# Performance work log

Measured on AMD Instinct MI355X. Metric: run time of the kernel, lower is better.

The kernel has to match this reference:

```python
import jax, jax.numpy as jnp
import numpy as np

B, S, DIM, H, HD, K, DEPTH = 2, 2048, 1024, 16, 64, 64, 8
SCALE = 1.0 / np.sqrt(HD)


def _build_cantor_routes(seq_len: int, k: int, depth: int) -> np.ndarray:
    # Vectorized version of CantorAttention._build_cantor_routes
    pos = np.arange(seq_len, dtype=np.float64)
    x = pos / max(1, seq_len - 1)
    x = np.clip(x, 1e-06, 1.0 - 1e-06)
    cantor = np.zeros(seq_len, dtype=np.float64)
    factor = 0.5
    for _ in range(depth):
        x = x * 3.0
        digit = np.floor(x)
        x = x - digit
        cantor += factor * (digit == 2.0)
        factor *= 0.5
    cantor = cantor.astype(np.float32)
    # k nearest positions in Cantor space for each position
    dist = np.abs(cantor[:, None] - cantor[None, :])  # [S, S]
    routes = np.argsort(dist, axis=1, kind='stable')[:, :k]  # [S, k]
    return routes.astype(np.int32)


def setup_inputs() -> dict:
    key = jax.random.key(0)
    k1, k2, k3, k4, k5 = jax.random.split(key, 5)
    s = 1.0 / np.sqrt(DIM)
    return {
        'x': jax.random.normal(k1, (B, S, DIM), dtype=jnp.float32),
        'w_qkv': jax.random.normal(k2, (3 * DIM, DIM), dtype=jnp.float32) * s,
        'b_qkv': jax.random.normal(k3, (3 * DIM,), dtype=jnp.float32) * 0.01,
        'w_out': jax.random.normal(k4, (DIM, DIM), dtype=jnp.float32) * s,
        'b_out': jax.random.normal(k5, (DIM,), dtype=jnp.float32) * 0.01,
        'routes': jnp.asarray(_build_cantor_routes(S, K, DEPTH)),
    }


def reference(x, w_qkv, b_qkv, w_out, b_out, routes):
    b, s, _ = x.shape
    # QKV projection (torch Linear: y = x @ W.T + b)
    qkv = x @ w_qkv.T + b_qkv                       # [B, S, 3*DIM]
    qkv = qkv.reshape(b, s, 3, H, HD).transpose(2, 0, 3, 1, 4)  # [3, B, H, S, HD]
    q, k, v = qkv[0], qkv[1], qkv[2]                # each [B, H, S, HD]
    # Gather k/v at Cantor neighbor routes: [B, H, S, K, HD]
    k_g = jnp.take(k, routes, axis=2)
    v_g = jnp.take(v, routes, axis=2)
    scores = jnp.einsum('bhqd,bhqkd->bhqk', q, k_g) * SCALE
    attn = jax.nn.softmax(scores, axis=-1)
    out = jnp.einsum('bhqk,bhqkd->bhqd', attn, v_g)  # [B, H, S, HD]
    out = out.transpose(0, 2, 1, 3).reshape(b, s, DIM)
    return out @ w_out.T + b_out
```

## Files before the change

kernel.cpp:

```cpp
#include <hip/hip_runtime.h>

#define BQ   2
#define SQ   2048
#define DIMQ 1024
#define HQ   16
#define HDQ  64
#define KQ   64
#define QKV_STRIDE (3 * DIMQ)

typedef __attribute__((ext_vector_type(8))) short short8;
typedef __attribute__((ext_vector_type(4))) float floatx4;

typedef const __attribute__((address_space(1))) unsigned short* gas_t;
typedef __attribute__((address_space(3))) unsigned short* las_t;

__device__ __forceinline__ unsigned short f2b(float f) {
    union { float f; unsigned int u; } x; x.f = f;
    unsigned int r = x.u + 0x7fffu + ((x.u >> 16) & 1u);
    return (unsigned short)(r >> 16);
}
__device__ __forceinline__ float b2f(unsigned short u) {
    union { unsigned int u; float f; } x; x.u = ((unsigned int)u) << 16;
    return x.f;
}

__global__ __launch_bounds__(256) void cast3_f32_bf16(const float* __restrict__ s0, unsigned short* __restrict__ d0, int n0,
                                                      const float* __restrict__ s1, unsigned short* __restrict__ d1, int n1,
                                                      const float* __restrict__ s2, unsigned short* __restrict__ d2, int n2) {
    int i = blockIdx.x * blockDim.x + threadIdx.x;
    const float* s; unsigned short* d;
    if (i < n0)                { s = s0; d = d0; }
    else if (i < n0 + n1)      { s = s1; d = d1; i -= n0; }
    else if (i < n0 + n1 + n2) { s = s2; d = d2; i -= n0 + n1; }
    else return;
    float4 v = ((const float4*)s)[i];
    ushort4 o;
    o.x = f2b(v.x); o.y = f2b(v.y); o.z = f2b(v.z); o.w = f2b(v.w);
    ((ushort4*)d)[i] = o;
}

template <int BM, int BN, typename CT>
__global__ __launch_bounds__(256) void gemm_bf16_nt(const unsigned short* __restrict__ A,
                                                    const unsigned short* __restrict__ B,
                                                    const float* __restrict__ bias,
                                                    CT* __restrict__ C,
                                                    int M, int N, int K) {
    constexpr int MI = BM / 32;
    constexpr int NJ = BN / 32;
    __shared__ unsigned short As[BM * 64];
    __shared__ unsigned short Bs[BN * 64];

    const int tid  = threadIdx.x;
    const int lane = tid & 63;
    const int wv   = tid >> 6;
    const int wm   = (wv >> 1) * (BM / 2);
    const int wn   = (wv & 1) * (BN / 2);
    const int fr   = lane & 15;
    const int fq   = lane >> 4;

    const int m0 = blockIdx.y * BM;
    const int n0 = blockIdx.x * BN;

    floatx4 acc[MI][NJ];
#pragma unroll
    for (int i = 0; i < MI; ++i)
#pragma unroll
        for (int j = 0; j < NJ; ++j) acc[i][j] = (floatx4)(0.f);

    const unsigned short* Ab = A + (size_t)m0 * K;
    const unsigned short* Bb = B + (size_t)n0 * K;

    for (int k0 = 0; k0 < K; k0 += 64) {
#pragma unroll
        for (int c = 0; c < (BM + BN) * 8; c += 256) {
            const int cc = c + tid;
            if (cc < BM * 8) {
                const int row = cc >> 3;
                const int kc  = ((cc & 7) ^ (row & 7)) << 3;
                __builtin_amdgcn_global_load_lds(
                    (gas_t)(Ab + (size_t)row * K + k0 + kc),
                    (las_t)&As[cc * 8], 16, 0, 0);
            } else {
                const int c2  = cc - BM * 8;
                const int row = c2 >> 3;
                const int kc  = ((c2 & 7) ^ (row & 7)) << 3;
                __builtin_amdgcn_global_load_lds(
                    (gas_t)(Bb + (size_t)row * K + k0 + kc),
                    (las_t)&Bs[c2 * 8], 16, 0, 0);
            }
        }
        __syncthreads();

#pragma unroll
        for (int ks = 0; ks < 2; ++ks) {
            short8 af[MI], bf[NJ];
#pragma unroll
            for (int i = 0; i < MI; ++i) {
                const int row = wm + i * 16 + fr;
                const int pos = (ks * 4 + fq) ^ (row & 7);
                af[i] = *(const short8*)&As[row * 64 + pos * 8];
            }
#pragma unroll
            for (int j = 0; j < NJ; ++j) {
                const int row = wn + j * 16 + fr;
                const int pos = (ks * 4 + fq) ^ (row & 7);
                bf[j] = *(const short8*)&Bs[row * 64 + pos * 8];
            }
#pragma unroll
            for (int i = 0; i < MI; ++i)
#pragma unroll
                for (int j = 0; j < NJ; ++j)
                    acc[i][j] = __builtin_amdgcn_mfma_f32_16x16x32_bf16(af[i], bf[j], acc[i][j], 0, 0, 0);
        }
        __syncthreads();
    }

    float bv[NJ];
#pragma unroll
    for (int j = 0; j < NJ; ++j) bv[j] = bias[n0 + wn + j * 16 + fr];
#pragma unroll
    for (int i = 0; i < MI; ++i) {
#pragma unroll
        for (int r = 0; r < 4; ++r) {
            const size_t row = (size_t)(m0 + wm + i * 16 + fq * 4 + r);
#pragma unroll
            for (int j = 0; j < NJ; ++j) {
                const float v = acc[i][j][r] + bv[j];
                if constexpr (sizeof(CT) == 2)
                    C[row * N + n0 + wn + j * 16 + fr] = (CT)f2b(v);
                else
                    C[row * N + n0 + wn + j * 16 + fr] = (CT)v;
            }
        }
    }
}

__global__ __launch_bounds__(256) void attn_kernel(const unsigned short* __restrict__ qkv,
                                                   const int* __restrict__ routes,
                                                   unsigned short* __restrict__ out) {
    __shared__ int   r_s[KQ];
    __shared__ float m_s[128], l_s[128];
    __shared__ float o_part[8][128];

    const int t  = threadIdx.x;
    const int id = blockIdx.x;
    const int bq = (id & 7) * 512 + (id >> 3);
    const int b  = bq >> 11;
    const int q  = bq & 2047;

    if (t < KQ) r_s[t] = routes[q * KQ + t];

    const int g  = t >> 7;
    const int th = t & 127;
    const int h  = th >> 3;
    const int d0 = (t & 7) * 8;

    float qf[8];
    {
        const short8 q8 = *(const short8*)&qkv[((size_t)bq * 3) * DIMQ + h * HDQ + d0];
#pragma unroll
        for (int e = 0; e < 8; ++e) qf[e] = b2f((unsigned short)q8[e]);
    }
    __syncthreads();

    const size_t baseK = ((size_t)b * SQ * 3 + 1) * DIMQ + h * HDQ + d0;
    const size_t baseV = ((size_t)b * SQ * 3 + 2) * DIMQ + h * HDQ + d0;

    float m = -1e30f, l = 0.f;
    float o[8];
#pragma unroll
    for (int e = 0; e < 8; ++e) o[e] = 0.f;

#pragma unroll 4
    for (int jj = 0; jj < KQ / 2; ++jj) {
        const int j = jj * 2 + g;
        const size_t roff = (size_t)r_s[j] * QKV_STRIDE;
        const short8 k8 = *(const short8*)&qkv[baseK + roff];
        const short8 v8 = *(const short8*)&qkv[baseV + roff];
        float p = 0.f;
#pragma unroll
        for (int e = 0; e < 8; ++e) p += qf[e] * b2f((unsigned short)k8[e]);
        p += __shfl_xor(p, 1, 64);
        p += __shfl_xor(p, 2, 64);
        p += __shfl_xor(p, 4, 64);
        const float s  = p * 0.125f;
        const float mn = fmaxf(m, s);
        const float al = __expf(m - mn);
        const float pe = __expf(s - mn);
        l = l * al + pe;
#pragma unroll
        for (int e = 0; e < 8; ++e) o[e] = o[e] * al + pe * b2f((unsigned short)v8[e]);
        m = mn;
    }

    if (g == 1) {
        m_s[th] = m; l_s[th] = l;
#pragma unroll
        for (int e = 0; e < 8; ++e) o_part[e][th] = o[e];
    }
    __syncthreads();
    if (g == 0) {
        const float m1 = m_s[th], l1 = l_s[th];
        const float mm = fmaxf(m, m1);
        const float a0 = __expf(m - mm);
        const float a1 = __expf(m1 - mm);
        const float inv = 1.0f / (l * a0 + l1 * a1);
        float oo[8];
#pragma unroll
        for (int e = 0; e < 8; ++e) oo[e] = (o[e] * a0 + o_part[e][th] * a1) * inv;
        ushort4 lo, hi;
        lo.x = f2b(oo[0]); lo.y = f2b(oo[1]); lo.z = f2b(oo[2]); lo.w = f2b(oo[3]);
        hi.x = f2b(oo[4]); hi.y = f2b(oo[5]); hi.z = f2b(oo[6]); hi.w = f2b(oo[7]);
        ushort4* dst = (ushort4*)&out[(size_t)bq * DIMQ + h * HDQ + d0];
        dst[0] = lo; dst[1] = hi;
    }
}

extern "C" void kernel_launch(void* const* d_in, const int* in_sizes, int n_in,
                              void* d_out, int out_size, void* d_ws, size_t ws_size,
                              hipStream_t stream) {
    const float* x      = (const float*)d_in[0];
    const float* w_qkv  = (const float*)d_in[1];
    const float* b_qkv  = (const float*)d_in[2];
    const float* w_out  = (const float*)d_in[3];
    const float* b_out  = (const float*)d_in[4];
    const int*   routes = (const int*)d_in[5];
    float* out = (float*)d_out;

    char* ws = (char*)d_ws;
    unsigned short* qkvb  = (unsigned short*)ws;
    unsigned short* xb    = (unsigned short*)(ws + 25165824);
    unsigned short* attnb = xb;
    unsigned short* wqb   = (unsigned short*)(ws + 33554432);
    unsigned short* wob   = (unsigned short*)(ws + 39845888);

    const int M = BQ * SQ;
    dim3 blk(256);

    {
        const int n0 = M * DIMQ / 4, n1 = 3 * DIMQ * DIMQ / 4, n2 = DIMQ * DIMQ / 4;
        cast3_f32_bf16<<<(n0 + n1 + n2 + 255) / 256, blk, 0, stream>>>(
            x, xb, n0, w_qkv, wqb, n1, w_out, wob, n2);
    }

    gemm_bf16_nt<128, 128, unsigned short><<<dim3(3 * DIMQ / 128, M / 128), blk, 0, stream>>>(
        xb, wqb, b_qkv, qkvb, M, 3 * DIMQ, DIMQ);

    attn_kernel<<<BQ * SQ, blk, 0, stream>>>(qkvb, routes, attnb);

    gemm_bf16_nt<128, 64, float><<<dim3(DIMQ / 64, M / 128), blk, 0, stream>>>(
        attnb, wob, b_out, out, M, DIMQ, DIMQ);
}
```

Before: 189.5 us.

## Order attention queries by Cantor rank and split softmax into two passes

Adds two small kernels that compute Cantor coordinates and a rank permutation of query positions on device. The attention kernel then processes queries in Cantor order, so neighbouring blocks gather overlapping K/V rows and cache reuse should improve. The online softmax is replaced by three phases: score computation into shared memory, a block-wide normalisation, then a weighted V sum. This removes the per-step rescaling exps but adds two block barriers and two extra kernel launches, one of which is an O(S^2) rank loop.

Measured after the change: 299.7 us. 1.58x slower.

```diff
diff --git a/kernel.cpp b/kernel.cpp
--- a/kernel.cpp
+++ b/kernel.cpp
@@ -22,6 +22,35 @@
 __device__ __forceinline__ float b2f(unsigned short u) {
     union { unsigned int u; float f; } x; x.u = ((unsigned int)u) << 16;
     return x.f;
+}
+
+__global__ __launch_bounds__(256) void cantor_vals(double* __restrict__ cant) {
+    const int q = blockIdx.x * 256 + threadIdx.x;
+    if (q >= SQ) return;
+    double x = (double)q / (double)(SQ - 1);
+    x = fmin(fmax(x, 1e-6), 1.0 - 1e-6);
+    double c = 0.0, factor = 0.5;
+    for (int d = 0; d < 8; ++d) {
+        x *= 3.0;
+        double digit = floor(x);
+        x -= digit;
+        if (digit == 2.0) c += factor;
+        factor *= 0.5;
+    }
+    cant[q] = c;
+}
+
+__global__ __launch_bounds__(256) void cantor_rank(const double* __restrict__ cant,
+                                                   int* __restrict__ qperm) {
+    const int q = blockIdx.x * 256 + threadIdx.x;
+    if (q >= SQ) return;
+    const double cq = cant[q];
+    int rank = 0;
+    for (int s = 0; s < SQ; ++s) {
+        const double cs = cant[s];
+        rank += (cs < cq) || (cs == cq && s < q);
+    }
+    qperm[rank] = q;
 }
 
 __global__ __launch_bounds__(256) void cast3_f32_bf16(const float* __restrict__ s0, unsigned short* __restrict__ d0, int n0,
@@ -137,16 +166,19 @@
 
 __global__ __launch_bounds__(256) void attn_kernel(const unsigned short* __restrict__ qkv,
                                                    const int* __restrict__ routes,
+                                                   const int* __restrict__ qperm,
                                                    unsigned short* __restrict__ out) {
+    __shared__ float s_s[HQ][KQ + 1];
     __shared__ int   r_s[KQ];
-    __shared__ float m_s[128], l_s[128];
     __shared__ float o_part[8][128];
 
     const int t  = threadIdx.x;
     const int id = blockIdx.x;
-    const int bq = (id & 7) * 512 + (id >> 3);
-    const int b  = bq >> 11;
-    const int q  = bq & 2047;
+    const int gri  = (id & 7) * 512 + (id >> 3);
+    const int b    = gri >> 11;
+    const int rank = gri & 2047;
+    const int q    = qperm[rank];
+    const int bq   = b * SQ + q;
 
     if (t < KQ) r_s[t] = routes[q * KQ + t];
 
@@ -166,51 +198,69 @@
     const size_t baseK = ((size_t)b * SQ * 3 + 1) * DIMQ + h * HDQ + d0;
     const size_t baseV = ((size_t)b * SQ * 3 + 2) * DIMQ + h * HDQ + d0;
 
-    float m = -1e30f, l = 0.f;
-    float o[8];
-#pragma unroll
-    for (int e = 0; e < 8; ++e) o[e] = 0.f;
-
-#pragma unroll 4
+#pragma unroll 8
     for (int jj = 0; jj < KQ / 2; ++jj) {
         const int j = jj * 2 + g;
-        const size_t roff = (size_t)r_s[j] * QKV_STRIDE;
-        const short8 k8 = *(const short8*)&qkv[baseK + roff];
-        const short8 v8 = *(const short8*)&qkv[baseV + roff];
+        const int r = r_s[j];
+        const short8 k8 = *(const short8*)&qkv[baseK + (size_t)r * QKV_STRIDE];
         float p = 0.f;
 #pragma unroll
         for (int e = 0; e < 8; ++e) p += qf[e] * b2f((unsigned short)k8[e]);
         p += __shfl_xor(p, 1, 64);
         p += __shfl_xor(p, 2, 64);
         p += __shfl_xor(p, 4, 64);
-        const float s  = p * 0.125f;
-        const float mn = fmaxf(m, s);
-        const float al = __expf(m - mn);
-        const float pe = __expf(s - mn);
-        l = l * al + pe;
-#pragma unroll
-        for (int e = 0; e < 8; ++e) o[e] = o[e] * al + pe * b2f((unsigned short)v8[e]);
-        m = mn;
-    }
-
+        if ((t & 7) == 0) s_s[h][j] = p * 0.125f;
+    }
+    __syncthreads();
+
+    {
+        const int lane = t & 63;
+        const int sh   = ((t >> 6) << 2) + (lane >> 4);
+        const int i    = lane & 15;
+        float v0 = s_s[sh][i], v1 = s_s[sh][i + 16], v2 = s_s[sh][i + 32], v3 = s_s[sh][i + 48];
+        float mx = fmaxf(fmaxf(v0, v1), fmaxf(v2, v3));
+        mx = fmaxf(mx, __shfl_xor(mx, 1, 64));
+        mx = fmaxf(mx, __shfl_xor(mx, 2, 64));
+        mx = fmaxf(mx, __shfl_xor(mx, 4, 64));
+        mx = fmaxf(mx, __shfl_xor(mx, 8, 64));
+        float e0 = __expf(v0 - mx), e1 = __expf(v1 - mx);
+        float e2 = __expf(v2 - mx), e3 = __expf(v3 - mx);
+        float sm = e0 + e1 + e2 + e3;
+        sm += __shfl_xor(sm, 1, 64);
+        sm += __shfl_xor(sm, 2, 64);
+        sm += __shfl_xor(sm, 4, 64);
+        sm += __shfl_xor(sm, 8, 64);
+        const float inv = 1.0f / sm;
+        s_s[sh][i]      = e0 * inv;
+        s_s[sh][i + 16] = e1 * inv;
+        s_s[sh][i + 32] = e2 * inv;
+        s_s[sh][i + 48] = e3 * inv;
+    }
+    __syncthreads();
+
+    float o[8];
+#pragma unroll
+    for (int e = 0; e < 8; ++e) o[e] = 0.f;
+#pragma unroll 8
+    for (int jj = 0; jj < KQ / 2; ++jj) {
+        const int   j = jj * 2 + g;
+        const int   r = r_s[j];
+        const float w = s_s[h][j];
+        const short8 v8 = *(const short8*)&qkv[baseV + (size_t)r * QKV_STRIDE];
+#pragma unroll
+        for (int e = 0; e < 8; ++e) o[e] += w * b2f((unsigned short)v8[e]);
+    }
     if (g == 1) {
-        m_s[th] = m; l_s[th] = l;
 #pragma unroll
         for (int e = 0; e < 8; ++e) o_part[e][th] = o[e];
     }
     __syncthreads();
     if (g == 0) {
-        const float m1 = m_s[th], l1 = l_s[th];
-        const float mm = fmaxf(m, m1);
-        const float a0 = __expf(m - mm);
-        const float a1 = __expf(m1 - mm);
-        const float inv = 1.0f / (l * a0 + l1 * a1);
-        float oo[8];
-#pragma unroll
-        for (int e = 0; e < 8; ++e) oo[e] = (o[e] * a0 + o_part[e][th] * a1) * inv;
         ushort4 lo, hi;
-        lo.x = f2b(oo[0]); lo.y = f2b(oo[1]); lo.z = f2b(oo[2]); lo.w = f2b(oo[3]);
-        hi.x = f2b(oo[4]); hi.y = f2b(oo[5]); hi.z = f2b(oo[6]); hi.w = f2b(oo[7]);
+        lo.x = f2b(o[0] + o_part[0][th]); lo.y = f2b(o[1] + o_part[1][th]);
+        lo.z = f2b(o[2] + o_part[2][th]); lo.w = f2b(o[3] + o_part[3][th]);
+        hi.x = f2b(o[4] + o_part[4][th]); hi.y = f2b(o[5] + o_part[5][th]);
+        hi.z = f2b(o[6] + o_part[6][th]); hi.w = f2b(o[7] + o_part[7][th]);
         ushort4* dst = (ushort4*)&out[(size_t)bq * DIMQ + h * HDQ + d0];
         dst[0] = lo; dst[1] = hi;
     }
@@ -233,9 +283,14 @@
     unsigned short* attnb = xb;
     unsigned short* wqb   = (unsigned short*)(ws + 33554432);
     unsigned short* wob   = (unsigned short*)(ws + 39845888);
+    double*         cant  = (double*)(ws + 41943040);
+    int*            qperm = (int*)(ws + 41959424);
 
     const int M = BQ * SQ;
     dim3 blk(256);
+
+    cantor_vals<<<SQ / 256, blk, 0, stream>>>(cant);
+    cantor_rank<<<SQ / 256, blk, 0, stream>>>(cant, qperm);
 
     {
         const int n0 = M * DIMQ / 4, n1 = 3 * DIMQ * DIMQ / 4, n2 = DIMQ * DIMQ / 4;
@@ -246,7 +301,7 @@
     gemm_bf16_nt<128, 128, unsigned short><<<dim3(3 * DIMQ / 128, M / 128), blk, 0, stream>>>(
         xb, wqb, b_qkv, qkvb, M, 3 * DIMQ, DIMQ);
 
-    attn_kernel<<<BQ * SQ, blk, 0, stream>>>(qkvb, routes, attnb);
+    attn_kernel<<<BQ * SQ, blk, 0, stream>>>(qkvb, routes, qperm, attnb);
 
     gemm_bf16_nt<128, 64, float><<<dim3(DIMQ / 64, M / 128), blk, 0, stream>>>(
         attnb, wob, b_out, out, M, DIMQ, DIMQ);
```
